# Optimization experiments

Hardware: AMD Instinct MI355X
Metric: run time of the kernel (lower is better)

## Reference

```python
import jax, jax.numpy as jnp
import numpy as np

B, T, D, DO = 8, 2048, 1024, 1024

def setup_inputs() -> dict:
    key = jax.random.key(0)
    ks = jax.random.split(key, 7)
    s = 1.0 / np.sqrt(D)
    return {
        "input_tensor": jax.random.normal(ks[0], (B, T, D), dtype=jnp.float32),
        "Wq": jax.random.uniform(ks[1], (D, D), jnp.float32, -s, s),
        "bq": jax.random.uniform(ks[2], (D,), jnp.float32, -s, s),
        "Wk": jax.random.uniform(ks[3], (D, D), jnp.float32, -s, s),
        "bk": jax.random.uniform(ks[4], (D,), jnp.float32, -s, s),
        "Wv": jax.random.uniform(ks[5], (D, DO), jnp.float32, -s, s),
        "bv": jax.random.uniform(ks[6], (DO,), jnp.float32, -s, s),
    }

def reference(input_tensor, Wq, bq, Wk, bk, Wv, bv):
    scale = jnp.sqrt(jnp.float32(input_tensor.shape[-1]))
    q = input_tensor @ Wq + bq            # [B,T,D]
    k = input_tensor @ Wk + bk            # [B,T,D]
    v = input_tensor @ Wv + bv            # [B,T,DO]
    scores = jnp.einsum('btd,bsd->bts', q, k) / scale  # [B,T,T]
    attn = jax.nn.softmax(scores, axis=-1)
    return jnp.einsum('bts,bso->bto', attn, v)         # [B,T,DO]
```

## Files before the change

### kernel.cpp

```cpp
#include <hip/hip_runtime.h>
#include <stdint.h>

typedef unsigned short u16;
typedef __attribute__((ext_vector_type(4))) float    floatx4;
typedef __attribute__((ext_vector_type(8))) __bf16   bf16x8;
typedef __attribute__((ext_vector_type(2))) unsigned int uintx2;
typedef __attribute__((ext_vector_type(4))) unsigned int uintx4;

__device__ inline u16 f2bf(float f) {
  unsigned int u = __builtin_bit_cast(unsigned int, f);
  u += 0x7fffu + ((u >> 16) & 1u);
  return (u16)(u >> 16);
}

#define GLD16(gsrc, ldst)                                                        \
  __builtin_amdgcn_global_load_lds(                                              \
      (__attribute__((address_space(1))) void*)(gsrc),                           \
      (__attribute__((address_space(3))) void*)(ldst), 16, 0, 0)

__global__ __launch_bounds__(256) void prep_kernel(const float* __restrict__ x,
                                                   const float* __restrict__ Wq,
                                                   const float* __restrict__ Wk,
                                                   const float* __restrict__ Wv,
                                                   u16* __restrict__ xb,
                                                   u16* __restrict__ WT) {
  const int z = blockIdx.z;
  const int tid = threadIdx.y * 32 + threadIdx.x;
  if (z >= 3) {
    long blk = (long)(z - 3) * 1024 + blockIdx.y * 32 + blockIdx.x;
    long i = (blk * 256 + tid) * 8;
    floatx4 a = *(const floatx4*)(x + i);
    floatx4 b = *(const floatx4*)(x + i + 4);
    uintx4 o;
    o[0] = (unsigned)f2bf(a[0]) | ((unsigned)f2bf(a[1]) << 16);
    o[1] = (unsigned)f2bf(a[2]) | ((unsigned)f2bf(a[3]) << 16);
    o[2] = (unsigned)f2bf(b[0]) | ((unsigned)f2bf(b[1]) << 16);
    o[3] = (unsigned)f2bf(b[2]) | ((unsigned)f2bf(b[3]) << 16);
    *(uintx4*)(xb + i) = o;
    return;
  }
  __shared__ float tile[32][33];
  const float* W = (z == 0) ? Wq : (z == 1) ? Wk : Wv;
  u16* dst = WT + (long)z * 1024 * 1024;
  int bx = blockIdx.x * 32, by = blockIdx.y * 32;
  int tx = threadIdx.x, ty = threadIdx.y;
  for (int i = 0; i < 32; i += 8)
    tile[ty + i][tx] = W[(long)(by + ty + i) * 1024 + bx + tx];
  __syncthreads();
  for (int i = 0; i < 32; i += 8)
    dst[(long)(bx + ty + i) * 1024 + by + tx] = f2bf(tile[tx][ty + i]);
}

#define BM 256
#define BN 256
#define BK 64

template <int MODE, int GN>
__global__ __launch_bounds__(512, 2)
void gemm_bt(const u16* __restrict__ Aall, const u16* __restrict__ Ball,
             void* __restrict__ Call, void* __restrict__ C2,
             const float* __restrict__ bias, const float* __restrict__ bias2,
             float* __restrict__ lsum,
             int M, int N, int K, long aStride, long bStride, long cStride) {
  __shared__ __align__(16) u16 As[2][BM * BK];
  __shared__ __align__(16) u16 Bs[2][BN * BK];

  const int z = blockIdx.z;
  const u16* A  = Aall + (long)z * aStride;
  const u16* Bt = Ball + (long)z * bStride;

  int m_idx, n_idx;
  if (GN > 0) {
    const int tiles_n = gridDim.x, tiles_m = gridDim.y;
    int bid = blockIdx.y * tiles_n + blockIdx.x;
    int per_group = GN * tiles_m;
    int g = bid / per_group;
    int rem = bid - g * per_group;
    n_idx = g * GN + rem % GN;
    m_idx = rem / GN;
  } else {
    m_idx = blockIdx.y; n_idx = blockIdx.x;
  }

  const int tid  = threadIdx.x;
  const int m0   = m_idx * BM;
  const int n0   = n_idx * BN;
  const int wave = tid >> 6;
  const int lane = tid & 63;
  const int wm   = (wave >> 2) * 128;
  const int wn   = (wave & 3) * 64;
  const int l15  = lane & 15;
  const int quad = lane >> 4;

  floatx4 acc[8][4];
  floatx4 zero = {0.f, 0.f, 0.f, 0.f};
#pragma unroll
  for (int i = 0; i < 8; ++i)
#pragma unroll
    for (int j = 0; j < 4; ++j) acc[i][j] = zero;

  int rows[4], cols[4];
#pragma unroll
  for (int i = 0; i < 4; ++i) {
    int ci = i * 512 + tid;
    int r = ci >> 3, sc = ci & 7;
    rows[i] = r; cols[i] = (sc ^ (r & 7)) * 8;
  }

  auto stageA = [&](int kt2, u16* dst, int b) {
    GLD16(A + (long)(m0 + rows[b]) * K + kt2 + cols[b], dst + (b * 512 + tid) * 8);
  };
  auto stageB = [&](int kt2, u16* dst, int b) {
    GLD16(Bt + (long)(n0 + rows[b]) * K + kt2 + cols[b], dst + (b * 512 + tid) * 8);
  };

  const int nt = K / BK;

  stageA(0, As[0], 0); stageA(0, As[0], 2);
  stageB(0, Bs[0], 0); stageB(0, Bs[0], 1);
  stageB(0, Bs[0], 2); stageB(0, Bs[0], 3);
  stageA(0, As[0], 1); stageA(0, As[0], 3);
  stageA(BK, As[1], 0); stageA(BK, As[1], 2);
  asm volatile("s_waitcnt vmcnt(2)" ::: "memory");
  __builtin_amdgcn_sched_barrier(0);
  __builtin_amdgcn_s_barrier();
  __builtin_amdgcn_sched_barrier(0);

  for (int t = 0; t < nt; ++t) {
    const int cur = t & 1;
    const u16* Ab = As[cur];
    const u16* Bb = Bs[cur];
    u16* Ac = As[cur];
    u16* An = As[cur ^ 1];
    u16* Bn = Bs[cur ^ 1];
    const int ktn = (t + 1) * BK;
    const bool st1 = (t + 1 < nt);
    const bool st2 = (t + 2 < nt);
    bf16x8 afA[4], afB[4], bfr[4];

#pragma unroll
    for (int mi = 0; mi < 4; ++mi) {
      int r = wm + mi * 16 + l15;
      afA[mi] = *(const bf16x8*)(Ab + (r * 8 + (quad ^ (r & 7))) * 8);
    }
#pragma unroll
    for (int ni = 0; ni < 4; ++ni) {
      int r = wn + ni * 16 + l15;
      bfr[ni] = *(const bf16x8*)(Bb + (r * 8 + (quad ^ (r & 7))) * 8);
    }
    if (st1) { stageB(ktn, Bn, 0); stageB(ktn, Bn, 1); }
    if (st1) asm volatile("s_waitcnt vmcnt(4)" ::: "memory");
    else     asm volatile("s_waitcnt vmcnt(0)" ::: "memory");
    asm volatile("s_waitcnt lgkmcnt(0)" ::: "memory");
    __builtin_amdgcn_sched_barrier(0);
    __builtin_amdgcn_s_barrier();
    __builtin_amdgcn_sched_barrier(0);
    __builtin_amdgcn_s_setprio(1);
#pragma unroll
    for (int mi = 0; mi < 4; ++mi)
#pragma unroll
      for (int ni = 0; ni < 4; ++ni)
        acc[mi][ni] = __builtin_amdgcn_mfma_f32_16x16x32_bf16(
            bfr[ni], afA[mi], acc[mi][ni], 0, 0, 0);
    __builtin_amdgcn_s_setprio(0);
    __builtin_amdgcn_sched_barrier(0);

#pragma unroll
    for (int mi = 0; mi < 4; ++mi) {
      int r = wm + (4 + mi) * 16 + l15;
      afB[mi] = *(const bf16x8*)(Ab + (r * 8 + (quad ^ (r & 7))) * 8);
    }
    if (st1) { stageB(ktn, Bn, 2); stageB(ktn, Bn, 3); }
    asm volatile("s_waitcnt lgkmcnt(0)" ::: "memory");
    __builtin_amdgcn_sched_barrier(0);
    __builtin_amdgcn_s_barrier();
    __builtin_amdgcn_sched_barrier(0);
    __builtin_amdgcn_s_setprio(1);
#pragma unroll
    for (int mi = 0; mi < 4; ++mi)
#pragma unroll
      for (int ni = 0; ni < 4; ++ni)
        acc[4 + mi][ni] = __builtin_amdgcn_mfma_f32_16x16x32_bf16(
            bfr[ni], afB[mi], acc[4 + mi][ni], 0, 0, 0);
    __builtin_amdgcn_s_setprio(0);
    __builtin_amdgcn_sched_barrier(0);

#pragma unroll
    for (int mi = 0; mi < 4; ++mi) {
      int r = wm + mi * 16 + l15;
      afA[mi] = *(const bf16x8*)(Ab + (r * 8 + ((4 + quad) ^ (r & 7))) * 8);
    }
#pragma unroll
    for (int ni = 0; ni < 4; ++ni) {
      int r = wn + ni * 16 + l15;
      bfr[ni] = *(const bf16x8*)(Bb + (r * 8 + ((4 + quad) ^ (r & 7))) * 8);
    }
    if (st1) { stageA(ktn, An, 1); stageA(ktn, An, 3); }
    asm volatile("s_waitcnt lgkmcnt(0)" ::: "memory");
    __builtin_amdgcn_sched_barrier(0);
    __builtin_amdgcn_s_barrier();
    __builtin_amdgcn_sched_barrier(0);
    __builtin_amdgcn_s_setprio(1);
#pragma unroll
    for (int mi = 0; mi < 4; ++mi)
#pragma unroll
      for (int ni = 0; ni < 4; ++ni)
        acc[mi][ni] = __builtin_amdgcn_mfma_f32_16x16x32_bf16(
            bfr[ni], afA[mi], acc[mi][ni], 0, 0, 0);
    __builtin_amdgcn_s_setprio(0);
    __builtin_amdgcn_sched_barrier(0);

#pragma unroll
    for (int mi = 0; mi < 4; ++mi) {
      int r = wm + (4 + mi) * 16 + l15;
      afB[mi] = *(const bf16x8*)(Ab + (r * 8 + ((4 + quad) ^ (r & 7))) * 8);
    }
    if (st2) { stageA(ktn + BK, Ac, 0); stageA(ktn + BK, Ac, 2); }
    if (st2)      asm volatile("s_waitcnt vmcnt(4)" ::: "memory");
    else if (st1) asm volatile("s_waitcnt vmcnt(2)" ::: "memory");
    asm volatile("s_waitcnt lgkmcnt(0)" ::: "memory");
    __builtin_amdgcn_sched_barrier(0);
    __builtin_amdgcn_s_barrier();
    __builtin_amdgcn_sched_barrier(0);
    __builtin_amdgcn_s_setprio(1);
#pragma unroll
    for (int mi = 0; mi < 4; ++mi)
#pragma unroll
      for (int ni = 0; ni < 4; ++ni)
        acc[4 + mi][ni] = __builtin_amdgcn_mfma_f32_16x16x32_bf16(
            bfr[ni], afB[mi], acc[4 + mi][ni], 0, 0, 0);
    __builtin_amdgcn_s_setprio(0);
    __builtin_amdgcn_sched_barrier(0);
  }

#pragma unroll
  for (int mi = 0; mi < 8; ++mi) {
    const int row = m0 + wm + mi * 16 + l15;
    if (MODE == 2) {
      u16* C = (u16*)Call + (long)z * cStride;
      float rs = 0.f;
#pragma unroll
      for (int ni = 0; ni < 4; ++ni) {
        int colb = n0 + wn + ni * 16 + quad * 4;
        floatx4 v = acc[mi][ni];
        float e0 = __expf(v[0] * 0.03125f), e1 = __expf(v[1] * 0.03125f);
        float e2 = __expf(v[2] * 0.03125f), e3 = __expf(v[3] * 0.03125f);
        rs += (e0 + e1) + (e2 + e3);
        uintx2 o;
        o[0] = (unsigned)f2bf(e0) | ((unsigned)f2bf(e1) << 16);
        o[1] = (unsigned)f2bf(e2) | ((unsigned)f2bf(e3) << 16);
        *(uintx2*)(C + (long)row * N + colb) = o;
      }
      rs += __shfl_xor(rs, 16);
      rs += __shfl_xor(rs, 32);
      if (quad == 0) atomicAdd(lsum + (long)z * 2048 + row, rs);
    } else if (MODE == 3) {
      float* C = (float*)Call + (long)z * cStride;
      float inv = 1.0f / lsum[(long)z * 2048 + row];
#pragma unroll
      for (int ni = 0; ni < 4; ++ni) {
        int colb = n0 + wn + ni * 16 + quad * 4;
        floatx4 v = acc[mi][ni];
        floatx4 o = {v[0] * inv, v[1] * inv, v[2] * inv, v[3] * inv};
        *(floatx4*)(C + (long)row * N + colb) = o;
      }
    } else if (MODE == 0) {
#pragma unroll
      for (int ni = 0; ni < 4; ++ni) {
        int colb = n0 + wn + ni * 16 + quad * 4;
        u16* C = (colb < 1024) ? (u16*)Call : (u16*)C2;
        const float* bp = (colb < 1024) ? bias + colb : bias2 + (colb - 1024);
        floatx4 b = *(const floatx4*)bp;
        floatx4 v = acc[mi][ni];
        uintx2 o;
        o[0] = (unsigned)f2bf(v[0] + b[0]) | ((unsigned)f2bf(v[1] + b[1]) << 16);
        o[1] = (unsigned)f2bf(v[2] + b[2]) | ((unsigned)f2bf(v[3] + b[3]) << 16);
        *(uintx2*)(C + (long)row * 1024 + (colb & 1023)) = o;
      }
    } else {
      u16* C = (u16*)Call;
      float b = bias[row];
#pragma unroll
      for (int ni = 0; ni < 4; ++ni) {
        int colb = n0 + wn + ni * 16 + quad * 4;
        long base = ((long)(colb >> 11) * 1024) * 2048 + (colb & 2047);
        floatx4 v = acc[mi][ni];
        uintx2 o;
        o[0] = (unsigned)f2bf(v[0] + b) | ((unsigned)f2bf(v[1] + b) << 16);
        o[1] = (unsigned)f2bf(v[2] + b) | ((unsigned)f2bf(v[3] + b) << 16);
        *(uintx2*)(C + base + (long)row * 2048) = o;
      }
    }
  }
}

extern "C" void kernel_launch(void* const* d_in, const int* in_sizes, int n_in,
                              void* d_out, int out_size, void* d_ws, size_t ws_size,
                              hipStream_t stream) {
  const float* x  = (const float*)d_in[0];
  const float* Wq = (const float*)d_in[1];
  const float* bq = (const float*)d_in[2];
  const float* Wk = (const float*)d_in[3];
  const float* bk = (const float*)d_in[4];
  const float* Wv = (const float*)d_in[5];
  const float* bv = (const float*)d_in[6];
  float* out = (float*)d_out;

  const long BT = 16384;
  u16* xb = (u16*)d_ws;
  u16* WT = xb + BT * 1024;
  u16* qb = WT + 3L * 1024 * 1024;
  u16* kb = qb + BT * 1024;
  u16* vT = kb + BT * 1024;
  u16* S  = vT + BT * 1024;
  float* lsum = (float*)(S + 8L * 2048 * 2048);

  hipMemsetAsync(lsum, 0, 8 * 2048 * sizeof(float), stream);

  prep_kernel<<<dim3(32, 32, 11), dim3(32, 8), 0, stream>>>(x, Wq, Wk, Wv, xb, WT);

  gemm_bt<0, 8><<<dim3(8, 64, 1), 512, 0, stream>>>(
      xb, WT, qb, kb, bq, bk, nullptr, 16384, 2048, 1024, 0, 0, 0);
  gemm_bt<1, 8><<<dim3(64, 4, 1), 512, 0, stream>>>(
      WT + 2L * 1024 * 1024, xb, vT, nullptr, bv, nullptr, nullptr,
      1024, 16384, 1024, 0, 0, 0);
  gemm_bt<2, 8><<<dim3(8, 8, 8), 512, 0, stream>>>(
      qb, kb, S, nullptr, nullptr, nullptr, lsum,
      2048, 2048, 1024, 2048L * 1024, 2048L * 1024, 2048L * 2048);
  gemm_bt<3, 4><<<dim3(4, 8, 8), 512, 0, stream>>>(
      S, vT, out, nullptr, nullptr, nullptr, lsum,
      2048, 1024, 2048, 2048L * 2048, 1024L * 2048, 2048L * 1024);
}
```

Before: 387.7 us.

## Remap workgroups across XCDs and restructure GEMM prefetch schedule

Workgroup IDs are now permuted so that consecutive logical tiles land on the same XCD (bid&7 interleave) before the grouped tile ordering, and the ungrouped path is removed so grouping always applies. The prologue no longer prefetches the next A tile. The main loop now stages the full next A tile within the same iteration, issues the LDS barrier before waiting on lgkmcnt, and changes the vmcnt thresholds. The intent is better L2 locality per XCD and a simpler double-buffer schedule, at the cost of a shorter prefetch distance for A. It also risks a correctness dependence on GN>0 and on the tile count being divisible by 8.

Result: no change. 381.1 us (-1.7%).

```diff
diff --git a/kernel.cpp b/kernel.cpp
--- a/kernel.cpp
+++ b/kernel.cpp
@@ -17,6 +17,8 @@
   __builtin_amdgcn_global_load_lds(                                              \
       (__attribute__((address_space(1))) void*)(gsrc),                           \
       (__attribute__((address_space(3))) void*)(ldst), 16, 0, 0)
+
+#define SB() __builtin_amdgcn_sched_barrier(0)
 
 __global__ __launch_bounds__(256) void prep_kernel(const float* __restrict__ x,
                                                    const float* __restrict__ Wq,
@@ -70,16 +72,17 @@
   const u16* Bt = Ball + (long)z * bStride;
 
   int m_idx, n_idx;
-  if (GN > 0) {
+  {
     const int tiles_n = gridDim.x, tiles_m = gridDim.y;
+    int nwg = tiles_n * tiles_m;
     int bid = blockIdx.y * tiles_n + blockIdx.x;
+    int qq = nwg >> 3;
+    int L = (bid & 7) * qq + (bid >> 3);
     int per_group = GN * tiles_m;
-    int g = bid / per_group;
-    int rem = bid - g * per_group;
+    int g = L / per_group;
+    int rem = L - g * per_group;
     n_idx = g * GN + rem % GN;
     m_idx = rem / GN;
-  } else {
-    m_idx = blockIdx.y; n_idx = blockIdx.x;
   }
 
   const int tid  = threadIdx.x;
@@ -116,26 +119,24 @@
 
   const int nt = K / BK;
 
-  stageA(0, As[0], 0); stageA(0, As[0], 2);
   stageB(0, Bs[0], 0); stageB(0, Bs[0], 1);
   stageB(0, Bs[0], 2); stageB(0, Bs[0], 3);
+  stageA(0, As[0], 0); stageA(0, As[0], 2);
   stageA(0, As[0], 1); stageA(0, As[0], 3);
-  stageA(BK, As[1], 0); stageA(BK, As[1], 2);
-  asm volatile("s_waitcnt vmcnt(2)" ::: "memory");
-  __builtin_amdgcn_sched_barrier(0);
+  SB();
+  asm volatile("s_waitcnt vmcnt(0)" ::: "memory");
+  SB();
   __builtin_amdgcn_s_barrier();
-  __builtin_amdgcn_sched_barrier(0);
+  SB();
 
   for (int t = 0; t < nt; ++t) {
     const int cur = t & 1;
     const u16* Ab = As[cur];
     const u16* Bb = Bs[cur];
-    u16* Ac = As[cur];
     u16* An = As[cur ^ 1];
     u16* Bn = Bs[cur ^ 1];
     const int ktn = (t + 1) * BK;
     const bool st1 = (t + 1 < nt);
-    const bool st2 = (t + 2 < nt);
     bf16x8 afA[4], afB[4], bfr[4];
 
 #pragma unroll
@@ -149,12 +150,13 @@
       bfr[ni] = *(const bf16x8*)(Bb + (r * 8 + (quad ^ (r & 7))) * 8);
     }
     if (st1) { stageB(ktn, Bn, 0); stageB(ktn, Bn, 1); }
-    if (st1) asm volatile("s_waitcnt vmcnt(4)" ::: "memory");
+    SB();
+    if (st1) asm volatile("s_waitcnt vmcnt(2)" ::: "memory");
     else     asm volatile("s_waitcnt vmcnt(0)" ::: "memory");
+    SB();
+    __builtin_amdgcn_s_barrier();
     asm volatile("s_waitcnt lgkmcnt(0)" ::: "memory");
-    __builtin_amdgcn_sched_barrier(0);
-    __builtin_amdgcn_s_barrier();
-    __builtin_amdgcn_sched_barrier(0);
+    SB();
     __builtin_amdgcn_s_setprio(1);
 #pragma unroll
     for (int mi = 0; mi < 4; ++mi)
@@ -163,7 +165,7 @@
         acc[mi][ni] = __builtin_amdgcn_mfma_f32_16x16x32_bf16(
             bfr[ni], afA[mi], acc[mi][ni], 0, 0, 0);
     __builtin_amdgcn_s_setprio(0);
-    __builtin_amdgcn_sched_barrier(0);
+    SB();
 
 #pragma unroll
     for (int mi = 0; mi < 4; ++mi) {
@@ -171,10 +173,10 @@
       afB[mi] = *(const bf16x8*)(Ab + (r * 8 + (quad ^ (r & 7))) * 8);
     }
     if (st1) { stageB(ktn, Bn, 2); stageB(ktn, Bn, 3); }
+    SB();
+    __builtin_amdgcn_s_barrier();
     asm volatile("s_waitcnt lgkmcnt(0)" ::: "memory");
-    __builtin_amdgcn_sched_barrier(0);
-    __builtin_amdgcn_s_barrier();
-    __builtin_amdgcn_sched_barrier(0);
+    SB();
     __builtin_amdgcn_s_setprio(1);
 #pragma unroll
     for (int mi = 0; mi < 4; ++mi)
@@ -183,7 +185,7 @@
         acc[4 + mi][ni] = __builtin_amdgcn_mfma_f32_16x16x32_bf16(
             bfr[ni], afB[mi], acc[4 + mi][ni], 0, 0, 0);
     __builtin_amdgcn_s_setprio(0);
-    __builtin_amdgcn_sched_barrier(0);
+    SB();
 
 #pragma unroll
     for (int mi = 0; mi < 4; ++mi) {
@@ -195,11 +197,11 @@
       int r = wn + ni * 16 + l15;
       bfr[ni] = *(const bf16x8*)(Bb + (r * 8 + ((4 + quad) ^ (r & 7))) * 8);
     }
-    if (st1) { stageA(ktn, An, 1); stageA(ktn, An, 3); }
+    if (st1) { stageA(ktn, An, 0); stageA(ktn, An, 2); }
+    SB();
+    __builtin_amdgcn_s_barrier();
     asm volatile("s_waitcnt lgkmcnt(0)" ::: "memory");
-    __builtin_amdgcn_sched_barrier(0);
-    __builtin_amdgcn_s_barrier();
-    __builtin_amdgcn_sched_barrier(0);
+    SB();
     __builtin_amdgcn_s_setprio(1);
 #pragma unroll
     for (int mi = 0; mi < 4; ++mi)
@@ -208,20 +210,20 @@
         acc[mi][ni] = __builtin_amdgcn_mfma_f32_16x16x32_bf16(
             bfr[ni], afA[mi], acc[mi][ni], 0, 0, 0);
     __builtin_amdgcn_s_setprio(0);
-    __builtin_amdgcn_sched_barrier(0);
+    SB();
 
 #pragma unroll
     for (int mi = 0; mi < 4; ++mi) {
       int r = wm + (4 + mi) * 16 + l15;
       afB[mi] = *(const bf16x8*)(Ab + (r * 8 + ((4 + quad) ^ (r & 7))) * 8);
     }
-    if (st2) { stageA(ktn + BK, Ac, 0); stageA(ktn + BK, Ac, 2); }
-    if (st2)      asm volatile("s_waitcnt vmcnt(4)" ::: "memory");
-    else if (st1) asm volatile("s_waitcnt vmcnt(2)" ::: "memory");
+    if (st1) { stageA(ktn, An, 1); stageA(ktn, An, 3); }
+    SB();
+    if (st1) asm volatile("s_waitcnt vmcnt(2)" ::: "memory");
+    SB();
+    __builtin_amdgcn_s_barrier();
     asm volatile("s_waitcnt lgkmcnt(0)" ::: "memory");
-    __builtin_amdgcn_sched_barrier(0);
-    __builtin_amdgcn_s_barrier();
-    __builtin_amdgcn_sched_barrier(0);
+    SB();
     __builtin_amdgcn_s_setprio(1);
 #pragma unroll
     for (int mi = 0; mi < 4; ++mi)
@@ -230,7 +232,7 @@
         acc[4 + mi][ni] = __builtin_amdgcn_mfma_f32_16x16x32_bf16(
             bfr[ni], afB[mi], acc[4 + mi][ni], 0, 0, 0);
     __builtin_amdgcn_s_setprio(0);
-    __builtin_amdgcn_sched_barrier(0);
+    SB();
   }
 
 #pragma unroll
```
